# Performance work log

Hardware: AMD Instinct MI355X
Metric: run time of the kernel (lower is better)

Reference implementation:

```python
import jax, jax.numpy as jnp
import numpy as np

D_MODEL = 1024
N_HEADS = 16
DEPTH = D_MODEL // N_HEADS
NEG_INF = -1.0e9


def setup_inputs() -> dict:
    key = jax.random.key(0)
    ks = jax.random.split(key, 11)
    B, S = 2, 2048
    xk = jax.random.normal(ks[0], (B, S, D_MODEL), jnp.float32)
    xq = jax.random.normal(ks[1], (B, S, D_MODEL), jnp.float32)
    xv = jax.random.normal(ks[2], (B, S, D_MODEL), jnp.float32)
    sc = 1.0 / np.sqrt(D_MODEL)
    wq = jax.random.normal(ks[3], (D_MODEL, D_MODEL), jnp.float32) * sc
    wk = jax.random.normal(ks[4], (D_MODEL, D_MODEL), jnp.float32) * sc
    wv = jax.random.normal(ks[5], (D_MODEL, D_MODEL), jnp.float32) * sc
    wo = jax.random.normal(ks[6], (D_MODEL, D_MODEL), jnp.float32) * sc
    bq = jnp.zeros((D_MODEL,), jnp.float32)
    bk = jnp.zeros((D_MODEL,), jnp.float32)
    bv = jnp.zeros((D_MODEL,), jnp.float32)
    bo = jnp.zeros((D_MODEL,), jnp.float32)
    return {"xk": xk, "xq": xq, "xv": xv, "wq": wq, "bq": bq, "wk": wk,
            "bk": bk, "wv": wv, "bv": bv, "wo": wo, "bo": bo}


def _split_heads(t):
    # [B, S, D] -> [B, H, S, depth]
    B, S, _ = t.shape
    return t.reshape(B, S, N_HEADS, DEPTH).transpose(0, 2, 1, 3)


def reference(xk, xq, xv, wq, bq, wk, bk, wv, bv, wo, bo):
    B, Sq, _ = xq.shape
    Sk = xk.shape[1]
    q = _split_heads(xq @ wq + bq)  # [B,H,Sq,d]
    k = _split_heads(xk @ wk + bk)  # [B,H,Sk,d]
    v = _split_heads(xv @ wv + bv)  # [B,H,Sk,d]
    logits = jnp.einsum('bhqd,bhkd->bhqk', q, k) / jnp.sqrt(
        jnp.asarray(DEPTH, q.dtype))
    # additive causal mask: (1 - lower_triangular) * -1e9
    causal = (1.0 - jnp.tril(jnp.ones((Sq, Sk), logits.dtype))) * NEG_INF
    logits = logits + causal[None, None, :, :]
    attn = jax.nn.softmax(logits, axis=-1)
    out = jnp.einsum('bhqk,bhkd->bhqd', attn, v)
    out = out.transpose(0, 2, 1, 3).reshape(B, Sq, D_MODEL)
    return out @ wo + bo
```

## Files before the change

### kernel.cpp

```cpp
#include <hip/hip_runtime.h>

typedef unsigned short u16;
typedef unsigned int u32;
typedef u16 u16x8 __attribute__((ext_vector_type(8)));
typedef u32 u32x4 __attribute__((ext_vector_type(4)));
typedef __bf16 bf16x8 __attribute__((ext_vector_type(8)));
typedef float f32x4 __attribute__((ext_vector_type(4)));
typedef float f32x16 __attribute__((ext_vector_type(16)));

#define DM 1024
#define SEQ 2048
#define BATCH 2
#define MROWS 4096

__device__ __forceinline__ u16 f2bf(float f) {
  unsigned int x = __builtin_bit_cast(unsigned int, f);
  x += 0x7fffu + ((x >> 16) & 1u);
  return (u16)(x >> 16);
}

__device__ __forceinline__ void gld16(const void* g, void* l) {
  __builtin_amdgcn_global_load_lds(
      (const __attribute__((address_space(1))) void*)g,
      (__attribute__((address_space(3))) void*)l, 16, 0, 0);
}

__device__ __forceinline__ u32 cvtpk_bf16(float lo, float hi) {
  u32 r;
  asm("v_cvt_pk_bf16_f32 %0, %1, %2" : "=v"(r) : "v"(lo), "v"(hi));
  return r;
}
__device__ __forceinline__ void pl32swap(u32& x, u32& y) {
  asm volatile("v_permlane32_swap_b32 %0, %1" : "+v"(x), "+v"(y));
}

struct TrArgs { const float* in[4]; u16* out[4]; };

__global__ __launch_bounds__(256) void transpose_w4(TrArgs a) {
  const float* __restrict__ in = a.in[blockIdx.z];
  u16* __restrict__ out = a.out[blockIdx.z];
  __shared__ u16 T[64][72];
  int r0 = blockIdx.y * 64, c0 = blockIdx.x * 64;
  int t = threadIdx.x;
  int r = t >> 3, cg = (t & 7) * 8;
#pragma unroll
  for (int p = 0; p < 2; p++) {
    const float* src = in + (size_t)(r0 + r + p * 32) * DM + c0 + cg;
    f32x4 x0 = *(const f32x4*)src;
    f32x4 x1 = *(const f32x4*)(src + 4);
    u16x8 v;
#pragma unroll
    for (int j = 0; j < 4; j++) { v[j] = f2bf(x0[j]); v[4 + j] = f2bf(x1[j]); }
    *(u16x8*)(&T[r + p * 32][cg]) = v;
  }
  __syncthreads();
#pragma unroll
  for (int p = 0; p < 2; p++) {
    int orow = r + p * 32;
    u16x8 v;
#pragma unroll
    for (int j = 0; j < 8; j++) v[j] = T[cg + j][orow];
    *(u16x8*)(out + (size_t)(c0 + orow) * DM + r0 + cg) = v;
  }
}

struct CastArgs { const float* in[3]; u16* out[3]; };

__global__ __launch_bounds__(256) void cast_x(CastArgs a) {
  const float* __restrict__ in = a.in[blockIdx.y];
  u16* __restrict__ out = a.out[blockIdx.y];
  size_t e = ((size_t)blockIdx.x * 256 + threadIdx.x) * 8;
  f32x4 a0 = *(const f32x4*)(in + e);
  f32x4 a1 = *(const f32x4*)(in + e + 4);
  u16x8 v;
#pragma unroll
  for (int j = 0; j < 4; j++) { v[j] = f2bf(a0[j]); v[4 + j] = f2bf(a1[j]); }
  *(u16x8*)(out + e) = v;
}

struct GemmArgs { const void* A[3]; const u16* WT[3]; const float* bias[3]; void* C[3]; };

template <int MT, int NT, bool AF32, bool OF32>
__global__ __launch_bounds__(256) void gemmT(GemmArgs g) {
  __shared__ __align__(16) u16 As[MT * 32 * 32];
  __shared__ __align__(16) u16 Bs[NT * 32 * 32];
  const int z = blockIdx.z;
  const u16* __restrict__ WT = g.WT[z];
  const int tid = threadIdx.x;
  const int lane = tid & 63, wave = tid >> 6;
  const int fr = lane & 15, kq = lane >> 4;
  const int mq = (wave >> 1) * (MT * 16), nq = (wave & 1) * (NT * 16);
  const int m0 = blockIdx.y * (MT * 32), n0 = blockIdx.x * (NT * 32);
  const int srow = tid >> 2;
  const int scA = ((tid & 3) ^ ((srow >> 1) & 3)) * 8;
  const int fco = ((kq ^ ((fr >> 1) & 3)) * 8);
  f32x4 acc[MT][NT] = {};

  for (int kk = 0; kk < DM; kk += 32) {
    __syncthreads();
    if constexpr (AF32) {
      const float* A = (const float*)g.A[z];
#pragma unroll
      for (int i = 0; i < MT / 2; i++) {
        const float* s0 = A + (size_t)(m0 + i * 64 + srow) * DM + kk + scA;
        f32x4 a0 = *(const f32x4*)s0, a1 = *(const f32x4*)(s0 + 4);
        u16x8 v;
#pragma unroll
        for (int j = 0; j < 4; j++) { v[j] = f2bf(a0[j]); v[4 + j] = f2bf(a1[j]); }
        *(u16x8*)(As + (i * 256 + tid) * 8) = v;
      }
    } else {
      const u16* A = (const u16*)g.A[z];
#pragma unroll
      for (int i = 0; i < MT / 2; i++)
        gld16(A + (size_t)(m0 + i * 64 + srow) * DM + kk + scA,
              As + (i * 256 + tid) * 8);
    }
#pragma unroll
    for (int i = 0; i < NT / 2; i++)
      gld16(WT + (size_t)(n0 + i * 64 + srow) * DM + kk + scA,
            Bs + (i * 256 + tid) * 8);
    __syncthreads();
    bf16x8 af[MT], bfr[NT];
#pragma unroll
    for (int mt = 0; mt < MT; mt++)
      af[mt] = __builtin_bit_cast(
          bf16x8, *(const u16x8*)(As + (mq + mt * 16 + fr) * 32 + fco));
#pragma unroll
    for (int nt = 0; nt < NT; nt++)
      bfr[nt] = __builtin_bit_cast(
          bf16x8, *(const u16x8*)(Bs + (nq + nt * 16 + fr) * 32 + fco));
#pragma unroll
    for (int mt = 0; mt < MT; mt++)
#pragma unroll
      for (int nt = 0; nt < NT; nt++)
        acc[mt][nt] =
            __builtin_amdgcn_mfma_f32_16x16x32_bf16(af[mt], bfr[nt], acc[mt][nt], 0, 0, 0);
  }
  const float* __restrict__ bias = g.bias[z];
#pragma unroll
  for (int nt = 0; nt < NT; nt++) {
    int col = n0 + nq + nt * 16 + fr;
    float bb = bias[col];
#pragma unroll
    for (int mt = 0; mt < MT; mt++)
#pragma unroll
      for (int r = 0; r < 4; r++) {
        int row = m0 + mq + mt * 16 + kq * 4 + r;
        float val = acc[mt][nt][r] + bb;
        if constexpr (OF32)
          ((float*)g.C[z])[(size_t)row * DM + col] = val;
        else
          ((u16*)g.C[z])[(size_t)row * DM + col] = f2bf(val);
      }
  }
}

#define KS 72
__global__ __launch_bounds__(256) void attn3(u16* __restrict__ Q,
                                             const u16* __restrict__ K,
                                             const u16* __restrict__ V) {
  __shared__ __align__(16) u16 Ksh[2][64 * 64];
  __shared__ __align__(16) u16 Vt[2][64 * KS];
  __shared__ float cmb[128][49];
  const int tid = threadIdx.x, wave = tid >> 6, lane = tid & 63;
  const int ql = lane & 31, hi = lane >> 5;
  const int pair = wave >> 1, w01 = wave & 1;
  const int b = blockIdx.x >> 4, h = blockIdx.x & 15;
  const int y = blockIdx.y;
  const float C1 = 0.125f * 1.44269504f;

  const int krow = tid >> 3;
  const int kcs = ((tid & 7) ^ (krow & 7)) * 8;
  const u16* Kg = K + (size_t)(b * SEQ + krow) * DM + h * 64 + kcs;
  const u16* Vg = V + (size_t)(b * SEQ + lane) * DM + h * 64 + wave * 16;

  int xsl[4];
#pragma unroll
  for (int f = 0; f < 4; f++) xsl[f] = ((2 * f + hi) ^ (ql & 7)) * 8;

  u16x8 onesu;
#pragma unroll
  for (int j = 0; j < 8; j++) onesu[j] = 0x3F80;
  const bf16x8 vones = __builtin_bit_cast(bf16x8, onesu);

  for (int pass = 0; pass < 2; pass++) {
    const int qt = pass ? y : 31 - y;

    bf16x8 qf[4];
    {
      size_t qr = (size_t)(b * SEQ + qt * 64 + w01 * 32 + ql) * DM + h * 64;
#pragma unroll
      for (int f = 0; f < 4; f++)
        qf[f] = __builtin_bit_cast(bf16x8,
                                   *(const u16x8*)(Q + qr + f * 16 + hi * 8));
    }

    f32x16 ov0 = {}, ov1 = {}, ovl = {};

    gld16(Kg, Ksh[0] + tid * 8);
    gld16(Kg + (size_t)32 * DM, Ksh[0] + (256 + tid) * 8);
    {
      u16x8 v0 = *(const u16x8*)(Vg);
      u16x8 v1 = *(const u16x8*)(Vg + 8);
#pragma unroll
      for (int j = 0; j < 8; j++) {
        Vt[0][(wave * 16 + j) * KS + lane] = v0[j];
        Vt[0][(wave * 16 + 8 + j) * KS + lane] = v1[j];
      }
    }
    __syncthreads();

    int cur = 0;
    for (int t = 0; t <= qt; t++) {
      const int nb = cur ^ 1;
      u16x8 nv0, nv1;
      const bool pf = (t < qt);
      if (pf) {
        size_t ro = (size_t)(t + 1) * 64 * DM;
        gld16(Kg + ro, Ksh[nb] + tid * 8);
        gld16(Kg + ro + (size_t)32 * DM, Ksh[nb] + (256 + tid) * 8);
        nv0 = *(const u16x8*)(Vg + ro);
        nv1 = *(const u16x8*)(Vg + ro + 8);
      }
      const u16* Kc = Ksh[cur];
      f32x16 s = {};
#pragma unroll
      for (int f = 0; f < 4; f++) {
        bf16x8 a0 = __builtin_bit_cast(
            bf16x8, *(const u16x8*)(Kc + (pair * 32 + ql) * 64 + xsl[f]));
        s = __builtin_amdgcn_mfma_f32_32x32x16_bf16(a0, qf[f], s, 0, 0, 0);
      }
      if (t == qt) {
        int qg = qt * 64 + w01 * 32 + ql;
        int kb = t * 64 + pair * 32 + 4 * hi;
#pragma unroll
        for (int r = 0; r < 16; r++) {
          int key = kb + (r & 3) + 8 * (r >> 2);
          if (key > qg) s[r] = -1e30f;
        }
      }
      const u16* Vc = Vt[cur];
      {
        float p[16];
#pragma unroll
        for (int r = 0; r < 16; r++)
          p[r] = __builtin_amdgcn_exp2f(s[r] * C1);
#pragma unroll
        for (int ss = 0; ss < 2; ss++) {
          u32 w0 = cvtpk_bf16(p[ss * 8 + 0], p[ss * 8 + 1]);
          u32 w1 = cvtpk_bf16(p[ss * 8 + 2], p[ss * 8 + 3]);
          u32 w2 = cvtpk_bf16(p[ss * 8 + 4], p[ss * 8 + 5]);
          u32 w3 = cvtpk_bf16(p[ss * 8 + 6], p[ss * 8 + 7]);
          pl32swap(w0, w2);
          pl32swap(w1, w3);
          u32x4 paw = {w0, w1, w2, w3};
          bf16x8 pa = __builtin_bit_cast(bf16x8, paw);
          const int kb2 = pair * 32 + ss * 16 + hi * 8;
          bf16x8 vb0 = __builtin_bit_cast(
              bf16x8, *(const u16x8*)(Vc + ql * KS + kb2));
          ov0 = __builtin_amdgcn_mfma_f32_32x32x16_bf16(pa, vb0, ov0, 0, 0, 0);
          bf16x8 vb1 = __builtin_bit_cast(
              bf16x8, *(const u16x8*)(Vc + (32 + ql) * KS + kb2));
          ov1 = __builtin_amdgcn_mfma_f32_32x32x16_bf16(pa, vb1, ov1, 0, 0, 0);
          ovl = __builtin_amdgcn_mfma_f32_32x32x16_bf16(pa, vones, ovl, 0, 0, 0);
        }
      }
      if (pf) {
#pragma unroll
        for (int j = 0; j < 8; j++) {
          Vt[nb][(wave * 16 + j) * KS + lane] = nv0[j];
          Vt[nb][(wave * 16 + 8 + j) * KS + lane] = nv1[j];
        }
      }
      __syncthreads();
      cur = nb;
    }
    if (pair == 1) {
      float* dst = cmb[w01 * 64 + lane];
#pragma unroll
      for (int r = 0; r < 16; r++) {
        dst[r] = ov0[r];
        dst[16 + r] = ov1[r];
        dst[32 + r] = ovl[r];
      }
    }
    __syncthreads();
    if (pair == 0) {
      const float* src = cmb[w01 * 64 + lane];
#pragma unroll
      for (int r = 0; r < 16; r++) {
        ov0[r] += src[r];
        ov1[r] += src[16 + r];
        ovl[r] += src[32 + r];
      }
      float rinv[16];
#pragma unroll
      for (int r = 0; r < 16; r++) rinv[r] = 1.0f / ovl[r];
#pragma unroll
      for (int r = 0; r < 16; r++) {
        int row = qt * 64 + w01 * 32 + (r & 3) + 8 * (r >> 2) + 4 * hi;
        size_t base = (size_t)(b * SEQ + row) * DM + h * 64 + ql;
        Q[base] = f2bf(ov0[r] * rinv[r]);
        Q[base + 32] = f2bf(ov1[r] * rinv[r]);
      }
    }
    __syncthreads();
  }
}

extern "C" void kernel_launch(void* const* d_in, const int* in_sizes, int n_in,
                              void* d_out, int out_size, void* d_ws,
                              size_t ws_size, hipStream_t stream) {
  const float* xk = (const float*)d_in[0];
  const float* xq = (const float*)d_in[1];
  const float* xv = (const float*)d_in[2];
  const float* wq = (const float*)d_in[3];
  const float* bq = (const float*)d_in[4];
  const float* wk = (const float*)d_in[5];
  const float* bk = (const float*)d_in[6];
  const float* wv = (const float*)d_in[7];
  const float* bv = (const float*)d_in[8];
  const float* wo = (const float*)d_in[9];
  const float* bo = (const float*)d_in[10];

  u16* Qb = (u16*)d_ws;
  u16* Kb = Qb + (size_t)MROWS * DM;
  u16* Vb = Kb + (size_t)MROWS * DM;
  u16* WTq = Vb + (size_t)MROWS * DM;
  u16* WTk = WTq + (size_t)DM * DM;
  u16* WTv = WTk + (size_t)DM * DM;
  u16* WTo = WTv + (size_t)DM * DM;
  u16* Xq = WTo + (size_t)DM * DM;
  u16* Xk = Xq + (size_t)MROWS * DM;
  u16* Xv = Xk + (size_t)MROWS * DM;
  const bool cast_path =
      ws_size >= ((size_t)(3 * 8 + 4 * 2 + 3 * 8)) * 1024 * 1024;

  dim3 blk(256);

  TrArgs tr;
  tr.in[0] = wq; tr.in[1] = wk; tr.in[2] = wv; tr.in[3] = wo;
  tr.out[0] = WTq; tr.out[1] = WTk; tr.out[2] = WTv; tr.out[3] = WTo;
  transpose_w4<<<dim3(16, 16, 4), blk, 0, stream>>>(tr);

  GemmArgs gq;
  gq.WT[0] = WTq; gq.WT[1] = WTk; gq.WT[2] = WTv;
  gq.bias[0] = bq; gq.bias[1] = bk; gq.bias[2] = bv;
  gq.C[0] = Qb; gq.C[1] = Kb; gq.C[2] = Vb;
  if (cast_path) {
    CastArgs ca;
    ca.in[0] = xq; ca.in[1] = xk; ca.in[2] = xv;
    ca.out[0] = Xq; ca.out[1] = Xk; ca.out[2] = Xv;
    cast_x<<<dim3(MROWS * DM / 2048, 3), blk, 0, stream>>>(ca);
    gq.A[0] = Xq; gq.A[1] = Xk; gq.A[2] = Xv;
    gemmT<4, 4, false, false>
        <<<dim3(DM / 128, MROWS / 128, 3), blk, 0, stream>>>(gq);
  } else {
    gq.A[0] = xq; gq.A[1] = xk; gq.A[2] = xv;
    gemmT<4, 4, true, false>
        <<<dim3(DM / 128, MROWS / 128, 3), blk, 0, stream>>>(gq);
  }

  attn3<<<dim3(BATCH * 16, 16), blk, 0, stream>>>(Qb, Kb, Vb);

  GemmArgs go;
  go.A[0] = Qb;  go.WT[0] = WTo; go.bias[0] = bo; go.C[0] = d_out;
  go.A[1] = Qb;  go.WT[1] = WTo; go.bias[1] = bo; go.C[1] = d_out;
  go.A[2] = Qb;  go.WT[2] = WTo; go.bias[2] = bo; go.C[2] = d_out;
  gemmT<2, 4, false, true>
      <<<dim3(DM / 128, MROWS / 64, 1), blk, 0, stream>>>(go);
}
```

Before: 223.6 us.

## Run both causal query tiles concurrently in 512-thread attention blocks sharing K/V loads

The attention kernel now uses 512 threads, with two groups of four waves that process the long and short query tiles of a block at the same time instead of in two sequential passes. Each K/V tile is loaded into shared memory once and consumed by both groups, halving per-wave load work and removing the second pass's reloading. The short tile's group writes its output mid-loop, and blockIdx.y is remapped so adjacent blocks pair heavy and light work. The cost is higher register and LDS pressure per block and idle waves in the short group once its tile finishes.

```diff
diff --git a/kernel.cpp b/kernel.cpp
--- a/kernel.cpp
+++ b/kernel.cpp
@@ -157,72 +157,84 @@
 }
 
 #define KS 72
-__global__ __launch_bounds__(256) void attn3(u16* __restrict__ Q,
-                                             const u16* __restrict__ K,
-                                             const u16* __restrict__ V) {
+__global__ __launch_bounds__(512, 4) void attn3(u16* __restrict__ Q,
+                                                const u16* __restrict__ K,
+                                                const u16* __restrict__ V) {
   __shared__ __align__(16) u16 Ksh[2][64 * 64];
   __shared__ __align__(16) u16 Vt[2][64 * KS];
   __shared__ float cmb[128][49];
   const int tid = threadIdx.x, wave = tid >> 6, lane = tid & 63;
   const int ql = lane & 31, hi = lane >> 5;
-  const int pair = wave >> 1, w01 = wave & 1;
+  const int grp = wave >> 2, w4 = wave & 3;
+  const int pair = w4 >> 1, w01 = w4 & 1;
   const int b = blockIdx.x >> 4, h = blockIdx.x & 15;
-  const int y = blockIdx.y;
+  const int by = blockIdx.y;
+  const int y = (by < 8) ? by : 23 - by;
+  const int qtA = 31 - y;
+  const int qt = grp ? y : qtA;
   const float C1 = 0.125f * 1.44269504f;
 
   const int krow = tid >> 3;
   const int kcs = ((tid & 7) ^ (krow & 7)) * 8;
   const u16* Kg = K + (size_t)(b * SEQ + krow) * DM + h * 64 + kcs;
-  const u16* Vg = V + (size_t)(b * SEQ + lane) * DM + h * 64 + wave * 16;
+  const u16* Vg = V + (size_t)(b * SEQ + lane) * DM + h * 64 + wave * 8;
 
   int xsl[4];
 #pragma unroll
   for (int f = 0; f < 4; f++) xsl[f] = ((2 * f + hi) ^ (ql & 7)) * 8;
+
+  bf16x8 qf[4];
+  {
+    size_t qr = (size_t)(b * SEQ + qt * 64 + w01 * 32 + ql) * DM + h * 64;
+#pragma unroll
+    for (int f = 0; f < 4; f++)
+      qf[f] = __builtin_bit_cast(bf16x8,
+                                 *(const u16x8*)(Q + qr + f * 16 + hi * 8));
+  }
 
   u16x8 onesu;
 #pragma unroll
   for (int j = 0; j < 8; j++) onesu[j] = 0x3F80;
   const bf16x8 vones = __builtin_bit_cast(bf16x8, onesu);
 
-  for (int pass = 0; pass < 2; pass++) {
-    const int qt = pass ? y : 31 - y;
-
-    bf16x8 qf[4];
-    {
-      size_t qr = (size_t)(b * SEQ + qt * 64 + w01 * 32 + ql) * DM + h * 64;
-#pragma unroll
-      for (int f = 0; f < 4; f++)
-        qf[f] = __builtin_bit_cast(bf16x8,
-                                   *(const u16x8*)(Q + qr + f * 16 + hi * 8));
-    }
-
-    f32x16 ov0 = {}, ov1 = {}, ovl = {};
-
-    gld16(Kg, Ksh[0] + tid * 8);
-    gld16(Kg + (size_t)32 * DM, Ksh[0] + (256 + tid) * 8);
-    {
-      u16x8 v0 = *(const u16x8*)(Vg);
-      u16x8 v1 = *(const u16x8*)(Vg + 8);
-#pragma unroll
-      for (int j = 0; j < 8; j++) {
-        Vt[0][(wave * 16 + j) * KS + lane] = v0[j];
-        Vt[0][(wave * 16 + 8 + j) * KS + lane] = v1[j];
-      }
-    }
-    __syncthreads();
-
-    int cur = 0;
-    for (int t = 0; t <= qt; t++) {
-      const int nb = cur ^ 1;
-      u16x8 nv0, nv1;
-      const bool pf = (t < qt);
-      if (pf) {
-        size_t ro = (size_t)(t + 1) * 64 * DM;
-        gld16(Kg + ro, Ksh[nb] + tid * 8);
-        gld16(Kg + ro + (size_t)32 * DM, Ksh[nb] + (256 + tid) * 8);
-        nv0 = *(const u16x8*)(Vg + ro);
-        nv1 = *(const u16x8*)(Vg + ro + 8);
-      }
+  f32x16 ov0 = {}, ov1 = {}, ovl = {};
+
+  gld16(Kg, Ksh[0] + tid * 8);
+  {
+    u16x8 v0 = *(const u16x8*)(Vg);
+#pragma unroll
+    for (int j = 0; j < 8; j++) Vt[0][(wave * 8 + j) * KS + lane] = v0[j];
+  }
+  __syncthreads();
+
+  int cur = 0;
+  for (int t = 0; t <= qtA; t++) {
+    const int nb = cur ^ 1;
+    u16x8 nv0;
+    const bool pf = (t < qtA);
+    if (pf) {
+      size_t ro = (size_t)(t + 1) * 64 * DM;
+      gld16(Kg + ro, Ksh[nb] + tid * 8);
+      nv0 = *(const u16x8*)(Vg + ro);
+    }
+    if (grp == 1 && pair == 0 && t == qt + 1) {
+      const float* src = cmb[w01 * 64 + lane];
+      float o0[16], o1[16], rl[16];
+#pragma unroll
+      for (int r = 0; r < 16; r++) {
+        o0[r] = ov0[r] + src[r];
+        o1[r] = ov1[r] + src[16 + r];
+        rl[r] = 1.0f / (ovl[r] + src[32 + r]);
+      }
+#pragma unroll
+      for (int r = 0; r < 16; r++) {
+        int row = qt * 64 + w01 * 32 + (r & 3) + 8 * (r >> 2) + 4 * hi;
+        size_t base = (size_t)(b * SEQ + row) * DM + h * 64 + ql;
+        Q[base] = f2bf(o0[r] * rl[r]);
+        Q[base + 32] = f2bf(o1[r] * rl[r]);
+      }
+    }
+    if (t <= qt) {
       const u16* Kc = Ksh[cur];
       f32x16 s = {};
 #pragma unroll
@@ -266,46 +278,49 @@
           ovl = __builtin_amdgcn_mfma_f32_32x32x16_bf16(pa, vones, ovl, 0, 0, 0);
         }
       }
-      if (pf) {
-#pragma unroll
-        for (int j = 0; j < 8; j++) {
-          Vt[nb][(wave * 16 + j) * KS + lane] = nv0[j];
-          Vt[nb][(wave * 16 + 8 + j) * KS + lane] = nv1[j];
+      if (grp == 1 && pair == 1 && t == qt) {
+        float* dst = cmb[w01 * 64 + lane];
+#pragma unroll
+        for (int r = 0; r < 16; r++) {
+          dst[r] = ov0[r];
+          dst[16 + r] = ov1[r];
+          dst[32 + r] = ovl[r];
         }
       }
-      __syncthreads();
-      cur = nb;
-    }
-    if (pair == 1) {
-      float* dst = cmb[w01 * 64 + lane];
-#pragma unroll
-      for (int r = 0; r < 16; r++) {
-        dst[r] = ov0[r];
-        dst[16 + r] = ov1[r];
-        dst[32 + r] = ovl[r];
-      }
+    }
+    if (pf) {
+#pragma unroll
+      for (int j = 0; j < 8; j++) Vt[nb][(wave * 8 + j) * KS + lane] = nv0[j];
     }
     __syncthreads();
-    if (pair == 0) {
-      const float* src = cmb[w01 * 64 + lane];
-#pragma unroll
-      for (int r = 0; r < 16; r++) {
-        ov0[r] += src[r];
-        ov1[r] += src[16 + r];
-        ovl[r] += src[32 + r];
-      }
-      float rinv[16];
-#pragma unroll
-      for (int r = 0; r < 16; r++) rinv[r] = 1.0f / ovl[r];
-#pragma unroll
-      for (int r = 0; r < 16; r++) {
-        int row = qt * 64 + w01 * 32 + (r & 3) + 8 * (r >> 2) + 4 * hi;
-        size_t base = (size_t)(b * SEQ + row) * DM + h * 64 + ql;
-        Q[base] = f2bf(ov0[r] * rinv[r]);
-        Q[base + 32] = f2bf(ov1[r] * rinv[r]);
-      }
-    }
-    __syncthreads();
+    cur = nb;
+  }
+  if (grp == 0 && pair == 1) {
+    float* dst = cmb[w01 * 64 + lane];
+#pragma unroll
+    for (int r = 0; r < 16; r++) {
+      dst[r] = ov0[r];
+      dst[16 + r] = ov1[r];
+      dst[32 + r] = ovl[r];
+    }
+  }
+  __syncthreads();
+  if (grp == 0 && pair == 0) {
+    const float* src = cmb[w01 * 64 + lane];
+    float rl[16];
+#pragma unroll
+    for (int r = 0; r < 16; r++) {
+      ov0[r] += src[r];
+      ov1[r] += src[16 + r];
+      rl[r] = 1.0f / (ovl[r] + src[32 + r]);
+    }
+#pragma unroll
+    for (int r = 0; r < 16; r++) {
+      int row = qt * 64 + w01 * 32 + (r & 3) + 8 * (r >> 2) + 4 * hi;
+      size_t base = (size_t)(b * SEQ + row) * DM + h * 64 + ql;
+      Q[base] = f2bf(ov0[r] * rl[r]);
+      Q[base + 32] = f2bf(ov1[r] * rl[r]);
+    }
   }
 }
 
@@ -362,7 +377,7 @@
         <<<dim3(DM / 128, MROWS / 128, 3), blk, 0, stream>>>(gq);
   }
 
-  attn3<<<dim3(BATCH * 16, 16), blk, 0, stream>>>(Qb, Kb, Vb);
+  attn3<<<dim3(BATCH * 16, 16), dim3(512), 0, stream>>>(Qb, Kb, Vb);
 
   GemmArgs go;
   go.A[0] = Qb;  go.WT[0] = WTo; go.bias[0] = bo; go.C[0] = d_out;
```

Result: slower. 264.0 us (+18.1%).
